# Optimization experiments

Hardware: AMD Instinct MI355X
Metric: run time of the kernel (lower is better)

Reference implementation:

```python
import jax, jax.numpy as jnp
import numpy as np
from jax import lax

NC = 10        # tess_size
EPS = 1e-07


def cpab_basis(nc):
    # Constraint matrix L @ Avees = 0, Avees = [a0,b0,a1,b1,...] per cell.
    # Continuity at interior knots x_i = i/nc, plus zero-boundary v(0)=v(1)=0.
    L = np.zeros((nc + 1, 2 * nc))
    for i in range(1, nc):
        xi = i / nc
        L[i - 1, 2 * (i - 1):2 * i] = [xi, 1.0]
        L[i - 1, 2 * i:2 * i + 2] = [-xi, -1.0]
    L[nc - 1, 1] = 1.0                      # v(0) = b_0 = 0
    L[nc, 2 * nc - 2:2 * nc] = [1.0, 1.0]   # v(1) = a_{nc-1} + b_{nc-1} = 0
    U, S, Vh = np.linalg.svd(L)
    rank = int((S > 1e-8 * S[0]).sum())
    return np.ascontiguousarray(Vh[rank:].T).astype(np.float32)  # (2*nc, nc-1)


def mlp(x1, W0, b0, W1, b1, W2, b2, W3, b3):
    h = jax.nn.relu(x1 @ W0 + b0)
    h = jax.nn.relu(h @ W1 + b1)
    h = jax.nn.relu(h @ W2 + b2)
    return h @ W3 + b3


def integrate_cpab(x, A, nc):
    # x: [N] in (0,1); A: [N, nc, 2] per-cell (slope a, intercept b).
    # Closed-form integration of dphi/dt = a_c*phi + b_c for t in [0,1],
    # walking across cells. Also accumulates s = integral of a(phi(t)) dt,
    # so dphi/dx = exp(s)  (space gradient of the transform).
    a_all = A[..., 0]
    b_all = A[..., 1]
    fnc = jnp.asarray(nc, x.dtype)
    c0 = jnp.clip(jnp.floor(x * nc).astype(jnp.int32), 0, nc - 1)

    def step(carry, _):
        phi, c, t, s, done = carry
        a = jnp.take_along_axis(a_all, c[:, None], 1)[:, 0]
        b = jnp.take_along_axis(b_all, c[:, None], 1)[:, 0]
        v = a * phi + b
        big = jnp.abs(a) > 1e-10
        a_safe = jnp.where(big, a, 1.0)
        # closed-form solution with remaining time t
        psi = jnp.where(big, (phi + b / a_safe) * jnp.exp(a * t) - b / a_safe,
                        phi + b * t)
        lo = c.astype(x.dtype) / fnc
        hi = (c + 1).astype(x.dtype) / fnc
        inside = (psi >= lo) & (psi <= hi)
        xc = jnp.where(v >= 0, hi, lo)          # boundary hit in flow direction
        vb = a * xc + b
        v_safe = jnp.where(v == 0, 1.0, v)
        ratio = jnp.maximum(vb / v_safe, 1e-30)
        t_hit = jnp.where(big, jnp.log(ratio) / a_safe, (xc - phi) / v_safe)
        act = ~done
        cross = act & ~inside
        s = s + jnp.where(act, a * jnp.where(inside, t, t_hit), 0.0)
        phi = jnp.where(cross, xc, jnp.where(act & inside, psi, phi))
        t = jnp.where(cross, t - t_hit, t)
        c = jnp.clip(jnp.where(cross, c + jnp.where(v >= 0, 1, -1), c), 0, nc - 1)
        done = done | inside
        return (phi, c, t, s, done), None

    init = (x, c0, jnp.ones_like(x), jnp.zeros_like(x),
            jnp.zeros(x.shape, bool))
    (phi, _, _, s, _), _ = lax.scan(step, init, None, length=nc + 1)
    return phi, jnp.exp(s)


def _forward(x, B, W0, b0, W1, b1, W2, b2, W3, b3):
    mask = jnp.array([1, 0])  # left=True
    x = jnp.clip(x, EPS, 1.0 - EPS)
    xm = x[:, mask]
    x1, x2 = xm[:, :1], xm[:, 1:]          # [N,1] each
    theta = mlp(x1, W0, b0, W1, b1, W2, b2, W3, b3)   # [N, nc-1]
    A = (theta @ B.T).reshape(-1, NC, 2)    # per-cell (a, b)
    z2, dz2 = integrate_cpab(x2[:, 0], A, NC)
    z = jnp.column_stack([x1[:, 0], z2])[:, mask]
    log_dz_dx = jnp.column_stack([jnp.zeros_like(x1[:, 0]),
                                  jnp.log(dz2)])[:, mask]
    return z, log_dz_dx


def setup_inputs() -> dict:
    key = jax.random.key(0)
    ks = jax.random.split(key, 9)
    N, H, D = 4_194_304, 10, NC - 1
    x = jax.random.uniform(ks[0], (N, 2), jnp.float32)
    sc = 0.5
    return {
        'x': x,
        'B': jnp.asarray(cpab_basis(NC)),
        'W0': jax.random.normal(ks[1], (1, H), jnp.float32) * sc,
        'b0': jax.random.normal(ks[2], (H,), jnp.float32) * 0.1,
        'W1': jax.random.normal(ks[3], (H, H), jnp.float32) * sc,
        'b1': jax.random.normal(ks[4], (H,), jnp.float32) * 0.1,
        'W2': jax.random.normal(ks[5], (H, H), jnp.float32) * sc,
        'b2': jax.random.normal(ks[6], (H,), jnp.float32) * 0.1,
        'W3': jax.random.normal(ks[7], (H, D), jnp.float32) * sc,
        'b3': jax.random.normal(ks[8], (D,), jnp.float32) * 0.1,
    }


def reference(x, B, W0, b0, W1, b1, W2, b2, W3, b3):
    return _forward(x, B, W0, b0, W1, b1, W2, b2, W3, b3)
```

## Files before the change

kernel.cpp:

```cpp
#include <hip/hip_runtime.h>
#include <math.h>

#define NCELL 10
#define TPTS  512
#define BLK   1024

__device__ __forceinline__ float satf(float v) {
    return fminf(fmaxf(v, -3.389e38f), 3.389e38f);
}

__global__ __launch_bounds__(256) void table_kernel(
    const float* __restrict__ B,
    const float* __restrict__ W0, const float* __restrict__ b0,
    const float* __restrict__ W1, const float* __restrict__ b1,
    const float* __restrict__ W2, const float* __restrict__ b2,
    const float* __restrict__ W3, const float* __restrict__ b3,
    float* __restrict__ tab, float lo, float hi, float dx)
{
    const int i = blockIdx.x * 256 + threadIdx.x;
    if (i >= TPTS) return;
    float x1 = fmaf((float)i, dx, lo);
    if (i == TPTS - 1) x1 = hi;

    float h0[10], h1[10], h2[10];
    #pragma unroll
    for (int j = 0; j < 10; ++j)
        h0[j] = fmaxf(fmaf(x1, W0[j], b0[j]), 0.0f);
    #pragma unroll
    for (int j = 0; j < 10; ++j) {
        float acc = b1[j];
        #pragma unroll
        for (int k = 0; k < 10; ++k) acc = fmaf(h0[k], W1[k * 10 + j], acc);
        h1[j] = fmaxf(acc, 0.0f);
    }
    #pragma unroll
    for (int j = 0; j < 10; ++j) {
        float acc = b2[j];
        #pragma unroll
        for (int k = 0; k < 10; ++k) acc = fmaf(h1[k], W2[k * 10 + j], acc);
        h2[j] = fmaxf(acc, 0.0f);
    }
    float theta[9];
    #pragma unroll
    for (int j = 0; j < 9; ++j) {
        float acc = b3[j];
        #pragma unroll
        for (int k = 0; k < 10; ++k) acc = fmaf(h2[k], W3[k * 9 + j], acc);
        theta[j] = acc;
    }
    float* row = tab + (size_t)i * 12;
    #pragma unroll
    for (int j = 1; j <= 9; ++j) {
        float aj = 0.f, bj = 0.f;
        #pragma unroll
        for (int q = 0; q < 9; ++q) {
            aj = fmaf(theta[q], B[(2 * j) * 9 + q], aj);
            bj = fmaf(theta[q], B[(2 * j + 1) * 9 + q], bj);
        }
        row[j - 1] = fmaf(aj, (float)j / 10.0f, bj);
    }
    row[9] = 0.0f; row[10] = 0.0f; row[11] = 0.0f;
}

__global__ __launch_bounds__(BLK) void cpab_kernel(
    const float* __restrict__ x,
    const float* __restrict__ tab,
    float* __restrict__ out, int N,
    float lo, float inv_dx)
{
    __shared__ float sTab[TPTS * 12];
    __shared__ float sN[NCELL + 1][BLK];

    const int tid = threadIdx.x;

    {
        const float4* g4 = reinterpret_cast<const float4*>(tab);
        float4* s4 = reinterpret_cast<float4*>(sTab);
        #pragma unroll
        for (int k = tid; k < TPTS * 3; k += BLK) s4[k] = g4[k];
    }
    __syncthreads();

    const int i = blockIdx.x * BLK + tid;
    if (i >= N) return;

    const float2 xv = reinterpret_cast<const float2*>(x)[i];
    const float hi_clip = 1.0f - 1e-7f;
    const float x2 = fminf(fmaxf(xv.x, 1e-7f), hi_clip);
    const float x1 = fminf(fmaxf(xv.y, 1e-7f), hi_clip);

    const float tt  = (x1 - lo) * inv_dx;
    const int  cell = min((int)tt, TPTS - 2);
    const float f   = tt - (float)cell;
    const float4* r = reinterpret_cast<const float4*>(sTab) + cell * 3;
    const float4 a0 = r[0], a1 = r[1], a2 = r[2];
    const float4 c0 = r[3], c1 = r[4], c2 = r[5];

    sN[0][tid]  = 0.0f;
    sN[1][tid]  = fmaf(f, c0.x - a0.x, a0.x);
    sN[2][tid]  = fmaf(f, c0.y - a0.y, a0.y);
    sN[3][tid]  = fmaf(f, c0.z - a0.z, a0.z);
    sN[4][tid]  = fmaf(f, c0.w - a0.w, a0.w);
    sN[5][tid]  = fmaf(f, c1.x - a1.x, a1.x);
    sN[6][tid]  = fmaf(f, c1.y - a1.y, a1.y);
    sN[7][tid]  = fmaf(f, c1.z - a1.z, a1.z);
    sN[8][tid]  = fmaf(f, c1.w - a1.w, a1.w);
    sN[9][tid]  = fmaf(f, c2.x - a2.x, a2.x);
    sN[NCELL][tid] = 0.0f;

    const float p10  = x2 * 10.0f;
    const int   cc0  = (int)p10;
    const float frac = p10 - (float)cc0;
    const float nc = sN[cc0][tid];
    const float nn = sN[cc0 + 1][tid];
    const float a0s = (nn - nc) * 10.0f;
    const float u0 = fmaf(nn - nc, frac, nc);
    const bool  right = (u0 >= 0.0f);
    const float d10   = right ? 10.0f : -10.0f;
    const int   dint  = right ? 1 : -1;

    float p  = x2;
    float u  = u0;
    float ru = __builtin_amdgcn_rcpf(u0);
    int   cn = cc0 + (right ? 1 : 0);
    float w  = right ? nn : nc;
    float t  = 1.0f;
    float a  = 0.0f, ra = 1.0f;
    bool  big = false;

    #pragma unroll 1
    for (int it = 0; ; ++it) {
        a   = (w - u) * d10;
        big = fabsf(a) > 1e-10f;
        ra  = __builtin_amdgcn_rcpf(big ? a : 1.0f);
        const float q  = w * ru;
        const float lg = __logf(q);
        const float xc = (float)cn * 0.1f;
        const float t_hit = big ? (lg * ra) : ((xc - p) * ru);
        if (!(t_hit < t) || it >= 11) break;
        t  -= t_hit;
        p   = xc;
        u   = w;
        ru  = __builtin_amdgcn_rcpf(w);
        cn += dint;
        w   = sN[cn][tid];
    }

    const float e   = __expf(a * t);
    float phi = big ? fmaf(u * ra, e - 1.0f, p) : fmaf(u, t, p);
    const float ru0 = __builtin_amdgcn_rcpf(u0);
    float ldz = __logf(fabsf(u * e * ru0));
    if (u0 == 0.0f) { phi = x2; ldz = a0s; }

    reinterpret_cast<float2*>(out)[i] = make_float2(satf(phi), x1);
    reinterpret_cast<float2*>(out + (size_t)2 * N)[i] = make_float2(satf(ldz), 0.0f);
}

extern "C" void kernel_launch(void* const* d_in, const int* in_sizes, int n_in,
                              void* d_out, int out_size, void* d_ws, size_t ws_size,
                              hipStream_t stream) {
    (void)n_in; (void)out_size; (void)ws_size;
    const float* x  = (const float*)d_in[0];
    const float* B  = (const float*)d_in[1];
    const float* W0 = (const float*)d_in[2];
    const float* b0 = (const float*)d_in[3];
    const float* W1 = (const float*)d_in[4];
    const float* b1 = (const float*)d_in[5];
    const float* W2 = (const float*)d_in[6];
    const float* b2 = (const float*)d_in[7];
    const float* W3 = (const float*)d_in[8];
    const float* b3 = (const float*)d_in[9];
    float* ws  = (float*)d_ws;
    float* out = (float*)d_out;

    const int N = in_sizes[0] / 2;
    const float lo = 1e-7f, hi = 1.0f - 1e-7f;
    const float dx = (hi - lo) / (float)(TPTS - 1);
    const float inv_dx = (float)(TPTS - 1) / (hi - lo);

    table_kernel<<<(TPTS + 255) / 256, 256, 0, stream>>>(
        B, W0, b0, W1, b1, W2, b2, W3, b3, ws, lo, hi, dx);
    cpab_kernel<<<(N + BLK - 1) / BLK, BLK, 0, stream>>>(
        x, ws, out, N, lo, inv_dx);
}
```

Before: 126.3 us.

## Store node table column-major and interpolate nodes on demand instead of per-thread LDS array

The precomputed node-velocity table is now stored transposed (9 rows of TPTS entries), and the main kernel no longer writes an 11-entry per-thread velocity array into shared memory. Instead each node value is interpolated lazily from the shared table when it is needed, including inside the cell-walk loop. This cuts shared memory use from roughly 68KB to 18KB, which can allow more blocks per CU, and removes eleven LDS stores per thread. The cost is two LDS reads plus an FMA per lookup inside the loop, and those reads are scattered by cell index, so bank conflicts are possible.

```diff
diff --git a/kernel.cpp b/kernel.cpp
--- a/kernel.cpp
+++ b/kernel.cpp
@@ -48,7 +48,6 @@
         for (int k = 0; k < 10; ++k) acc = fmaf(h2[k], W3[k * 9 + j], acc);
         theta[j] = acc;
     }
-    float* row = tab + (size_t)i * 12;
     #pragma unroll
     for (int j = 1; j <= 9; ++j) {
         float aj = 0.f, bj = 0.f;
@@ -57,9 +56,8 @@
             aj = fmaf(theta[q], B[(2 * j) * 9 + q], aj);
             bj = fmaf(theta[q], B[(2 * j + 1) * 9 + q], bj);
         }
-        row[j - 1] = fmaf(aj, (float)j / 10.0f, bj);
+        tab[(j - 1) * TPTS + i] = fmaf(aj, (float)j / 10.0f, bj);
     }
-    row[9] = 0.0f; row[10] = 0.0f; row[11] = 0.0f;
 }
 
 __global__ __launch_bounds__(BLK) void cpab_kernel(
@@ -68,16 +66,15 @@
     float* __restrict__ out, int N,
     float lo, float inv_dx)
 {
-    __shared__ float sTab[TPTS * 12];
-    __shared__ float sN[NCELL + 1][BLK];
+    __shared__ float sT[9 * TPTS];
 
     const int tid = threadIdx.x;
 
     {
         const float4* g4 = reinterpret_cast<const float4*>(tab);
-        float4* s4 = reinterpret_cast<float4*>(sTab);
+        float4* s4 = reinterpret_cast<float4*>(sT);
         #pragma unroll
-        for (int k = tid; k < TPTS * 3; k += BLK) s4[k] = g4[k];
+        for (int k = tid; k < 9 * TPTS / 4; k += BLK) s4[k] = g4[k];
     }
     __syncthreads();
 
@@ -92,27 +89,21 @@
     const float tt  = (x1 - lo) * inv_dx;
     const int  cell = min((int)tt, TPTS - 2);
     const float f   = tt - (float)cell;
-    const float4* r = reinterpret_cast<const float4*>(sTab) + cell * 3;
-    const float4 a0 = r[0], a1 = r[1], a2 = r[2];
-    const float4 c0 = r[3], c1 = r[4], c2 = r[5];
 
-    sN[0][tid]  = 0.0f;
-    sN[1][tid]  = fmaf(f, c0.x - a0.x, a0.x);
-    sN[2][tid]  = fmaf(f, c0.y - a0.y, a0.y);
-    sN[3][tid]  = fmaf(f, c0.z - a0.z, a0.z);
-    sN[4][tid]  = fmaf(f, c0.w - a0.w, a0.w);
-    sN[5][tid]  = fmaf(f, c1.x - a1.x, a1.x);
-    sN[6][tid]  = fmaf(f, c1.y - a1.y, a1.y);
-    sN[7][tid]  = fmaf(f, c1.z - a1.z, a1.z);
-    sN[8][tid]  = fmaf(f, c1.w - a1.w, a1.w);
-    sN[9][tid]  = fmaf(f, c2.x - a2.x, a2.x);
-    sN[NCELL][tid] = 0.0f;
+    const float* base = sT + cell;
+    auto node = [&](int j) -> float {
+        const int jj = (min(max(j, 1), 9) - 1) * TPTS;
+        const float v0 = base[jj];
+        const float v1 = base[jj + 1];
+        const float v  = fmaf(f, v1 - v0, v0);
+        return (j >= 1 && j <= 9) ? v : 0.0f;
+    };
 
     const float p10  = x2 * 10.0f;
     const int   cc0  = (int)p10;
     const float frac = p10 - (float)cc0;
-    const float nc = sN[cc0][tid];
-    const float nn = sN[cc0 + 1][tid];
+    const float nc = node(cc0);
+    const float nn = node(cc0 + 1);
     const float a0s = (nn - nc) * 10.0f;
     const float u0 = fmaf(nn - nc, frac, nc);
     const bool  right = (u0 >= 0.0f);
@@ -143,7 +134,7 @@
         u   = w;
         ru  = __builtin_amdgcn_rcpf(w);
         cn += dint;
-        w   = sN[cn][tid];
+        w   = node(cn);
     }
 
     const float e   = __expf(a * t);
```

Measured after the change: 121.8 us. 3.6% less time.
